# Performance work log

Measured on AMD Instinct MI355X. Metric: run time of the kernel, lower is better.

## Reference

```python
import jax, jax.numpy as jnp
import numpy as np

N = 16384
K = 4096  # codebook_size
D = 512   # embedding_dim
COMMITMENT_COST = 0.25


def setup_inputs() -> dict:
    key = jax.random.key(0)
    kz, kc = jax.random.split(key)
    z = jax.random.normal(kz, (N, D), dtype=jnp.float32)
    # nn.Embedding weight init: uniform(-1/K, 1/K)
    codebook = jax.random.uniform(kc, (K, D), dtype=jnp.float32,
                                  minval=-1.0 / K, maxval=1.0 / K)
    return {"z": z, "codebook": codebook}


def reference(z, codebook):
    # squared L2 distances: [N, K]
    dists = (jnp.sum(z * z, axis=1, keepdims=True)
             + jnp.sum(codebook * codebook, axis=1)
             - 2.0 * jnp.matmul(z, codebook.T))
    idx = jnp.argmin(dists, axis=1)                 # [N]
    z_q = codebook[idx]                             # gather == one-hot @ codebook
    # straight-through estimator
    z_q_ste = z + jax.lax.stop_gradient(z_q - z)
    commitment_loss = jnp.mean((jax.lax.stop_gradient(z) - z_q) ** 2)
    codebook_loss = jnp.mean((z - jax.lax.stop_gradient(z_q)) ** 2)
    loss = codebook_loss + COMMITMENT_COST * commitment_loss
    encoding_indices = idx[:, None]                 # [N, 1] to match torch shape
    return (z_q_ste, encoding_indices, loss)
```

## Files before the change

### kernel.cpp

```cpp
#include <hip/hip_runtime.h>
#include <math.h>

#define N_ROWS 16384
#define K_CODES 4096
#define D_DIM 512
#define NCHUNK 8
#define KCHUNK (K_CODES / NCHUNK)
#define MARGIN 2.5e-3f
#define CAND_CAP 1024

typedef unsigned int uint32;
typedef unsigned short u16t;
typedef __attribute__((ext_vector_type(8))) short short8;
typedef __attribute__((ext_vector_type(4))) float f32x4;

__device__ __forceinline__ float fmul_(float a, float b) { return __fmul_rn(a, b); }
__device__ __forceinline__ float fadd_(float a, float b) { return __fadd_rn(a, b); }

__global__ void rownorm_np_kernel(const float* __restrict__ src, int nrows,
                                  float* __restrict__ out) {
    int gid = blockIdx.x * blockDim.x + threadIdx.x;
    int row = gid >> 2;
    int blk = gid & 3;
    if (row >= nrows) return;
    const float4* p = (const float4*)(src + (size_t)row * D_DIM + blk * 128);
    float4 v0 = p[0], v1 = p[1];
    float r0 = fmul_(v0.x, v0.x), r1 = fmul_(v0.y, v0.y);
    float r2 = fmul_(v0.z, v0.z), r3 = fmul_(v0.w, v0.w);
    float r4 = fmul_(v1.x, v1.x), r5 = fmul_(v1.y, v1.y);
    float r6 = fmul_(v1.z, v1.z), r7 = fmul_(v1.w, v1.w);
#pragma unroll
    for (int i = 1; i < 16; i++) {
        float4 w0 = p[2 * i], w1 = p[2 * i + 1];
        r0 = fadd_(r0, fmul_(w0.x, w0.x));
        r1 = fadd_(r1, fmul_(w0.y, w0.y));
        r2 = fadd_(r2, fmul_(w0.z, w0.z));
        r3 = fadd_(r3, fmul_(w0.w, w0.w));
        r4 = fadd_(r4, fmul_(w1.x, w1.x));
        r5 = fadd_(r5, fmul_(w1.y, w1.y));
        r6 = fadd_(r6, fmul_(w1.z, w1.z));
        r7 = fadd_(r7, fmul_(w1.w, w1.w));
    }
    float s = fadd_(fadd_(fadd_(r0, r1), fadd_(r2, r3)),
                    fadd_(fadd_(r4, r5), fadd_(r6, r7)));
    float u = __shfl_down(s, 1, 64);
    float t = fadd_(s, u);
    float w = __shfl_down(t, 2, 64);
    float tot = fadd_(t, w);
    if (blk == 0) out[row] = tot;
}

__device__ __forceinline__ u16t f2bf(float x) {
    uint32 u = __float_as_uint(x);
    return (u16t)((u + 0x7fffu + ((u >> 16) & 1u)) >> 16);
}
__global__ void cvt_bf16_kernel(const float* __restrict__ src,
                                u16t* __restrict__ dst, int n4) {
    int i = blockIdx.x * blockDim.x + threadIdx.x;
    if (i >= n4) return;
    float4 v = ((const float4*)src)[i];
    ushort4 o;
    o.x = f2bf(v.x); o.y = f2bf(v.y); o.z = f2bf(v.z); o.w = f2bf(v.w);
    ((ushort4*)dst)[i] = o;
}

#define STS 136

__global__ __launch_bounds__(256) void score_gemm_kernel(
    const u16t* __restrict__ zb, const u16t* __restrict__ cbb,
    const float* __restrict__ cnorm, u16t* __restrict__ scores) {
    __shared__ alignas(16) u16t Ab[128 * 32];
    __shared__ alignas(16) u16t Bb[128 * 32];
    __shared__ alignas(16) u16t stile[128 * STS];

    const int t = threadIdx.x;
    const int bx = blockIdx.x;
    const int by = blockIdx.y;
    const int row0 = by * 128, k0 = bx * KCHUNK;
    const int w = t >> 6, lane = t & 63;
    const int wx = w & 1, wy = w >> 1;
    const int l15 = lane & 15, quad = lane >> 4;

    for (int kt = 0; kt < 4; kt++) {
        f32x4 acc[4][4];
#pragma unroll
        for (int i = 0; i < 4; i++)
#pragma unroll
            for (int j = 0; j < 4; j++) acc[i][j] = (f32x4){0.f, 0.f, 0.f, 0.f};

        for (int dt = 0; dt < 16; dt++) {
            __syncthreads();
#pragma unroll
            for (int q = 0; q < 2; q++) {
                int s = q * 256 + t;
                const u16t* ga = zb + (size_t)(row0 + (s >> 2)) * D_DIM + dt * 32 + (s & 3) * 8;
                __builtin_amdgcn_global_load_lds(
                    (const __attribute__((address_space(1))) void*)ga,
                    (__attribute__((address_space(3))) void*)((char*)Ab + q * 4096 + w * 1024),
                    16, 0, 0);
                const u16t* gb = cbb + (size_t)(k0 + kt * 128 + (s >> 2)) * D_DIM + dt * 32 + (s & 3) * 8;
                __builtin_amdgcn_global_load_lds(
                    (const __attribute__((address_space(1))) void*)gb,
                    (__attribute__((address_space(3))) void*)((char*)Bb + q * 4096 + w * 1024),
                    16, 0, 0);
            }
            __syncthreads();
            short8 a[4], b[4];
#pragma unroll
            for (int i = 0; i < 4; i++)
                a[i] = *(const short8*)((char*)Ab + (wy * 64 + i * 16 + l15) * 64 + quad * 16);
#pragma unroll
            for (int j = 0; j < 4; j++)
                b[j] = *(const short8*)((char*)Bb + (wx * 64 + j * 16 + l15) * 64 + quad * 16);
#pragma unroll
            for (int i = 0; i < 4; i++)
#pragma unroll
                for (int j = 0; j < 4; j++)
                    acc[i][j] = __builtin_amdgcn_mfma_f32_16x16x32_bf16(a[i], b[j], acc[i][j], 0, 0, 0);
        }
#pragma unroll
        for (int j = 0; j < 4; j++) {
            int cl = wx * 64 + j * 16 + l15;
            float cn = cnorm[k0 + kt * 128 + cl];
#pragma unroll
            for (int i = 0; i < 4; i++) {
#pragma unroll
                for (int r = 0; r < 4; r++) {
                    int rl = wy * 64 + i * 16 + quad * 4 + r;
                    float s = fmaf(-2.f, acc[i][j][r], cn);
                    stile[rl * STS + cl] = f2bf(s);
                }
            }
        }
        __syncthreads();
        for (int idx = t; idx < 128 * 16; idx += 256) {
            int row = idx >> 4, seg = idx & 15;
            short8 v = *(const short8*)&stile[row * STS + seg * 8];
            *(short8*)(scores + (size_t)(row0 + row) * K_CODES + k0 + kt * 128 + seg * 8) = v;
        }
    }
}

__global__ __launch_bounds__(256) void scan_refine_kernel(
    const u16t* __restrict__ scores,
    const float* __restrict__ z, const float* __restrict__ cb,
    const float* __restrict__ zz, const float* __restrict__ cnorm,
    float* __restrict__ out_zq, float* __restrict__ out_idx,
    float* __restrict__ rowsum) {
    __shared__ float smin[256];
    __shared__ int clist[CAND_CAP];
    __shared__ int cnt;
    __shared__ float wbv[4];
    __shared__ int wbi[4];
    __shared__ float red[256];
    __shared__ int bcast;

    const int row = blockIdx.x;
    const int t = threadIdx.x;
    const int w = t >> 6, lane = t & 63;

    if (t == 0) cnt = 0;

    const u16t* srow = scores + (size_t)row * K_CODES + t * 16;
    short8 sv0 = *(const short8*)(srow);
    short8 sv1 = *(const short8*)(srow + 8);
    float f[16];
#pragma unroll
    for (int e = 0; e < 8; e++) {
        f[e]     = __uint_as_float(((uint32)(u16t)sv0[e]) << 16);
        f[e + 8] = __uint_as_float(((uint32)(u16t)sv1[e]) << 16);
    }
    float m = f[0];
#pragma unroll
    for (int e = 1; e < 16; e++) m = fminf(m, f[e]);
    smin[t] = m;
    __syncthreads();
    for (int st = 128; st; st >>= 1) {
        if (t < st) smin[t] = fminf(smin[t], smin[t + st]);
        __syncthreads();
    }
    const float thr = smin[0] + MARGIN;

#pragma unroll
    for (int e = 0; e < 16; e++) {
        if (f[e] <= thr) {
            int pos = atomicAdd(&cnt, 1);
            if (pos < CAND_CAP) clist[pos] = t * 16 + e;
        }
    }
    __syncthreads();
    const int C = cnt < CAND_CAP ? cnt : CAND_CAP;

    const float* zr = z + (size_t)row * D_DIM;
    float4 z0 = *(const float4*)(zr + lane * 8);
    float4 z1 = *(const float4*)(zr + lane * 8 + 4);
    float zzr = zz[row];

    float bv = 3.4e38f;
    int bi = 0x7fffffff;
    for (int ci = w; ci < C; ci += 4) {
        int k = clist[ci];
        const float* cr = cb + (size_t)k * D_DIM;
        float4 c0 = *(const float4*)(cr + lane * 8);
        float4 c1 = *(const float4*)(cr + lane * 8 + 4);
        float d = fmul_(z0.x, c0.x);
        d = fmaf(z0.y, c0.y, d); d = fmaf(z0.z, c0.z, d); d = fmaf(z0.w, c0.w, d);
        d = fmaf(z1.x, c1.x, d); d = fmaf(z1.y, c1.y, d);
        d = fmaf(z1.z, c1.z, d); d = fmaf(z1.w, c1.w, d);
#pragma unroll
        for (int off = 1; off < 64; off <<= 1)
            d = fadd_(d, __shfl_xor(d, off, 64));
        float dist = fmaf(-2.f, d, fadd_(zzr, cnorm[k]));
        if (dist < bv || (dist == bv && k < bi)) { bv = dist; bi = k; }
    }
    if (lane == 0) { wbv[w] = bv; wbi[w] = bi; }
    __syncthreads();
    if (t == 0) {
        float B = wbv[0]; int I = wbi[0];
#pragma unroll
        for (int i = 1; i < 4; i++) {
            float v = wbv[i]; int ii = wbi[i];
            if (v < B || (v == B && ii < I)) { B = v; I = ii; }
        }
        bcast = I;
        out_idx[row] = (float)I;
    }
    __syncthreads();
    const int K = bcast;
    const float* cq = cb + (size_t)K * D_DIM;
    float2 zv2 = *(const float2*)(zr + t * 2);
    float2 cv2 = *(const float2*)(cq + t * 2);
    float2 o;
    o.x = fadd_(zv2.x, __fsub_rn(cv2.x, zv2.x));
    o.y = fadd_(zv2.y, __fsub_rn(cv2.y, zv2.y));
    *(float2*)(out_zq + (size_t)row * D_DIM + t * 2) = o;
    float dx = zv2.x - cv2.x, dy = zv2.y - cv2.y;
    red[t] = dx * dx + dy * dy;
    __syncthreads();
    for (int st = 128; st; st >>= 1) {
        if (t < st) red[t] += red[t + st];
        __syncthreads();
    }
    if (t == 0) rowsum[row] = red[0];
}

__global__ void loss_kernel(const float* __restrict__ rowsum,
                            float* __restrict__ out_loss) {
    __shared__ float sm[256];
    float s = 0.f;
    for (int i = threadIdx.x; i < N_ROWS; i += 256) s += rowsum[i];
    sm[threadIdx.x] = s;
    __syncthreads();
    for (int st = 128; st; st >>= 1) {
        if (threadIdx.x < st) sm[threadIdx.x] += sm[threadIdx.x + st];
        __syncthreads();
    }
    if (threadIdx.x == 0)
        *out_loss = 1.25f * sm[0] / (float)(N_ROWS * D_DIM);
}

#define BM 128
#define BN 128
#define BK 16
#define TM 8
#define TN 8

__global__ __launch_bounds__(256, 4) void vq_argmin_kernel(
    const float* __restrict__ z, const float* __restrict__ cb,
    const float* __restrict__ zz, const float* __restrict__ cnorm,
    float* __restrict__ pval, int* __restrict__ pidx) {
    __shared__ float As[BK][BM + 4];
    __shared__ float Bs[BK][BN + 4];
    __shared__ float rv[BM][17];
    __shared__ int   ri[BM][17];

    const int bx = blockIdx.x;
    const int by = blockIdx.y;
    const int row0 = by * BM;
    const int k0 = bx * KCHUNK;
    const int t = threadIdx.x;
    const int tx = t & 15;
    const int ty = t >> 4;

    float minv[TM];
    int   mini[TM];
#pragma unroll
    for (int i = 0; i < TM; i++) { minv[i] = 3.4e38f; mini[i] = 0; }
    float zrow[TM];
#pragma unroll
    for (int i = 0; i < TM; i++) zrow[i] = zz[row0 + ty * TM + i];
    const int sr = t >> 1;
    const int sdq = (t & 1) * 8;

    for (int kt = 0; kt < KCHUNK / BN; kt++) {
        const int col0 = k0 + kt * BN;
        float acc[TM][TN];
#pragma unroll
        for (int i = 0; i < TM; i++)
#pragma unroll
            for (int j = 0; j < TN; j++) acc[i][j] = 0.f;
        for (int dt = 0; dt < D_DIM; dt += BK) {
            {
                const float* src = z + (size_t)(row0 + sr) * D_DIM + dt + sdq;
                float4 v0 = *(const float4*)(src);
                float4 v1 = *(const float4*)(src + 4);
                As[sdq + 0][sr] = v0.x; As[sdq + 1][sr] = v0.y;
                As[sdq + 2][sr] = v0.z; As[sdq + 3][sr] = v0.w;
                As[sdq + 4][sr] = v1.x; As[sdq + 5][sr] = v1.y;
                As[sdq + 6][sr] = v1.z; As[sdq + 7][sr] = v1.w;
                const float* srcb = cb + (size_t)(col0 + sr) * D_DIM + dt + sdq;
                float4 w0 = *(const float4*)(srcb);
                float4 w1 = *(const float4*)(srcb + 4);
                Bs[sdq + 0][sr] = w0.x; Bs[sdq + 1][sr] = w0.y;
                Bs[sdq + 2][sr] = w0.z; Bs[sdq + 3][sr] = w0.w;
                Bs[sdq + 4][sr] = w1.x; Bs[sdq + 5][sr] = w1.y;
                Bs[sdq + 6][sr] = w1.z; Bs[sdq + 7][sr] = w1.w;
            }
            __syncthreads();
#pragma unroll
            for (int d = 0; d < BK; d++) {
                float a[TM], b[TN];
#pragma unroll
                for (int i = 0; i < TM; i++) a[i] = As[d][ty * TM + i];
#pragma unroll
                for (int j = 0; j < TN; j++) b[j] = Bs[d][tx * TN + j];
#pragma unroll
                for (int i = 0; i < TM; i++)
#pragma unroll
                    for (int j = 0; j < TN; j++)
                        acc[i][j] = fmaf(a[i], b[j], acc[i][j]);
            }
            __syncthreads();
        }
#pragma unroll
        for (int j = 0; j < TN; j++) {
            const int col = col0 + tx * TN + j;
            const float cn = cnorm[col];
#pragma unroll
            for (int i = 0; i < TM; i++) {
                float s1 = fadd_(zrow[i], cn);
                float s = fmaf(-2.f, acc[i][j], s1);
                if (s < minv[i]) { minv[i] = s; mini[i] = col; }
            }
        }
    }
#pragma unroll
    for (int i = 0; i < TM; i++) {
        rv[ty * TM + i][tx] = minv[i];
        ri[ty * TM + i][tx] = mini[i];
    }
    __syncthreads();
    if (t < BM) {
        float bv = rv[t][0];
        int   bi = ri[t][0];
#pragma unroll
        for (int x = 1; x < 16; x++) {
            float v = rv[t][x]; int ii = ri[t][x];
            if (v < bv || (v == bv && ii < bi)) { bv = v; bi = ii; }
        }
        pval[(size_t)(row0 + t) * NCHUNK + bx] = bv;
        pidx[(size_t)(row0 + t) * NCHUNK + bx] = bi;
    }
}

__global__ void finalize_kernel(const float* __restrict__ z,
                                const float* __restrict__ cb,
                                const float* __restrict__ pval,
                                const int* __restrict__ pidx,
                                float* __restrict__ out_zq,
                                float* __restrict__ out_idx,
                                float* __restrict__ rowsum) {
    int row = (blockIdx.x * blockDim.x + threadIdx.x) >> 6;
    int lane = threadIdx.x & 63;
    if (row >= N_ROWS) return;
    float bv = pval[(size_t)row * NCHUNK];
    int   bi = pidx[(size_t)row * NCHUNK];
#pragma unroll
    for (int c = 1; c < NCHUNK; c++) {
        float v = pval[(size_t)row * NCHUNK + c];
        int  ii = pidx[(size_t)row * NCHUNK + c];
        if (v < bv || (v == bv && ii < bi)) { bv = v; bi = ii; }
    }
    const float4* zr = (const float4*)(z + (size_t)row * D_DIM);
    const float4* cr = (const float4*)(cb + (size_t)bi * D_DIM);
    float4* orow = (float4*)(out_zq + (size_t)row * D_DIM);
    float s = 0.f;
#pragma unroll
    for (int i = 0; i < 2; i++) {
        float4 zv = zr[i * 64 + lane];
        float4 cv = cr[i * 64 + lane];
        float4 o;
        o.x = fadd_(zv.x, __fsub_rn(cv.x, zv.x));
        o.y = fadd_(zv.y, __fsub_rn(cv.y, zv.y));
        o.z = fadd_(zv.z, __fsub_rn(cv.z, zv.z));
        o.w = fadd_(zv.w, __fsub_rn(cv.w, zv.w));
        orow[i * 64 + lane] = o;
        float dx = zv.x - cv.x, dy = zv.y - cv.y;
        float dz = zv.z - cv.z, dw = zv.w - cv.w;
        s += dx * dx + dy * dy + dz * dz + dw * dw;
    }
#pragma unroll
    for (int off = 32; off; off >>= 1) s += __shfl_down(s, off, 64);
    if (lane == 0) {
        rowsum[row] = s;
        out_idx[row] = (float)bi;
    }
}

extern "C" void kernel_launch(void* const* d_in, const int* in_sizes, int n_in,
                              void* d_out, int out_size, void* d_ws, size_t ws_size,
                              hipStream_t stream) {
    const float* z  = (const float*)d_in[0];
    const float* cb = (const float*)d_in[1];
    float* out      = (float*)d_out;
    float* out_zq   = out;
    float* out_idx  = out + (size_t)N_ROWS * D_DIM;
    float* out_loss = out_idx + N_ROWS;

    float* zz     = (float*)d_ws;
    float* cnorm  = zz + N_ROWS;
    float* rowsum = cnorm + K_CODES;
    u16t*  z_bf   = (u16t*)(rowsum + N_ROWS);
    u16t*  cb_bf  = z_bf + (size_t)N_ROWS * D_DIM;
    u16t*  scores = cb_bf + (size_t)K_CODES * D_DIM;
    const size_t WS_NEEDED = (size_t)(N_ROWS + K_CODES + N_ROWS) * 4
                           + (size_t)N_ROWS * D_DIM * 2
                           + (size_t)K_CODES * D_DIM * 2
                           + (size_t)N_ROWS * K_CODES * 2;

    if (ws_size >= WS_NEEDED) {
        cvt_bf16_kernel<<<(N_ROWS * D_DIM / 4 + 255) / 256, 256, 0, stream>>>(z, z_bf, N_ROWS * D_DIM / 4);
        cvt_bf16_kernel<<<(K_CODES * D_DIM / 4 + 255) / 256, 256, 0, stream>>>(cb, cb_bf, K_CODES * D_DIM / 4);
        rownorm_np_kernel<<<(N_ROWS * 4) / 256, 256, 0, stream>>>(z, N_ROWS, zz);
        rownorm_np_kernel<<<(K_CODES * 4) / 256, 256, 0, stream>>>(cb, K_CODES, cnorm);

        dim3 g1(NCHUNK, N_ROWS / 128);
        score_gemm_kernel<<<g1, 256, 0, stream>>>(z_bf, cb_bf, cnorm, scores);
        scan_refine_kernel<<<N_ROWS, 256, 0, stream>>>(scores, z, cb, zz, cnorm,
                                                       out_zq, out_idx, rowsum);
        loss_kernel<<<1, 256, 0, stream>>>(rowsum, out_loss);
    } else {
        float* pval = rowsum + N_ROWS;
        int*   pidx = (int*)(pval + (size_t)N_ROWS * NCHUNK);
        rownorm_np_kernel<<<(N_ROWS * 4) / 256, 256, 0, stream>>>(z, N_ROWS, zz);
        rownorm_np_kernel<<<(K_CODES * 4) / 256, 256, 0, stream>>>(cb, K_CODES, cnorm);
        dim3 g2(NCHUNK, N_ROWS / BM);
        vq_argmin_kernel<<<g2, 256, 0, stream>>>(z, cb, zz, cnorm, pval, pidx);
        finalize_kernel<<<N_ROWS / 4, 256, 0, stream>>>(z, cb, pval, pidx,
                                                        out_zq, out_idx, rowsum);
        loss_kernel<<<1, 256, 0, stream>>>(rowsum, out_loss);
    }
}
```

Baseline: 287.5 us.

## Fuse bf16 conversion into rownorm, remap GEMM blocks per XCD, wave-per-row refine

Merges the bf16 conversion kernels into the row-norm kernel so each input is read once. The score GEMM uses a 1-D grid remapped so each XCD gets a contiguous block of tiles for L2 reuse, and halves its score staging tile by writing out in two 64-row halves. The refine kernel now assigns one row per wave and uses ballot/shuffle candidate enumeration instead of shared-memory atomics and block barriers. The GEMM adds extra syncs per tile, and the refine loop runs serially within each wave.

```diff
diff --git a/kernel.cpp b/kernel.cpp
--- a/kernel.cpp
+++ b/kernel.cpp
@@ -7,7 +7,6 @@
 #define NCHUNK 8
 #define KCHUNK (K_CODES / NCHUNK)
 #define MARGIN 2.5e-3f
-#define CAND_CAP 1024
 
 typedef unsigned int uint32;
 typedef unsigned short u16t;
@@ -17,14 +16,31 @@
 __device__ __forceinline__ float fmul_(float a, float b) { return __fmul_rn(a, b); }
 __device__ __forceinline__ float fadd_(float a, float b) { return __fadd_rn(a, b); }
 
-__global__ void rownorm_np_kernel(const float* __restrict__ src, int nrows,
-                                  float* __restrict__ out) {
+__device__ __forceinline__ u16t f2bf(float x) {
+    uint32 u = __float_as_uint(x);
+    return (u16t)((u + 0x7fffu + ((u >> 16) & 1u)) >> 16);
+}
+__device__ __forceinline__ float bf2f(u16t b) {
+    return __uint_as_float(((uint32)b) << 16);
+}
+
+__global__ void rownorm_cvt_kernel(const float* __restrict__ src, int nrows,
+                                   float* __restrict__ out,
+                                   u16t* __restrict__ bf) {
     int gid = blockIdx.x * blockDim.x + threadIdx.x;
     int row = gid >> 2;
     int blk = gid & 3;
     if (row >= nrows) return;
-    const float4* p = (const float4*)(src + (size_t)row * D_DIM + blk * 128);
+    const size_t base = (size_t)row * D_DIM + blk * 128;
+    const float4* p = (const float4*)(src + base);
     float4 v0 = p[0], v1 = p[1];
+    if (bf) {
+        ushort4 o0, o1;
+        o0.x = f2bf(v0.x); o0.y = f2bf(v0.y); o0.z = f2bf(v0.z); o0.w = f2bf(v0.w);
+        o1.x = f2bf(v1.x); o1.y = f2bf(v1.y); o1.z = f2bf(v1.z); o1.w = f2bf(v1.w);
+        *(ushort4*)(bf + base) = o0;
+        *(ushort4*)(bf + base + 4) = o1;
+    }
     float r0 = fmul_(v0.x, v0.x), r1 = fmul_(v0.y, v0.y);
     float r2 = fmul_(v0.z, v0.z), r3 = fmul_(v0.w, v0.w);
     float r4 = fmul_(v1.x, v1.x), r5 = fmul_(v1.y, v1.y);
@@ -32,6 +48,13 @@
 #pragma unroll
     for (int i = 1; i < 16; i++) {
         float4 w0 = p[2 * i], w1 = p[2 * i + 1];
+        if (bf) {
+            ushort4 o0, o1;
+            o0.x = f2bf(w0.x); o0.y = f2bf(w0.y); o0.z = f2bf(w0.z); o0.w = f2bf(w0.w);
+            o1.x = f2bf(w1.x); o1.y = f2bf(w1.y); o1.z = f2bf(w1.z); o1.w = f2bf(w1.w);
+            *(ushort4*)(bf + base + i * 8) = o0;
+            *(ushort4*)(bf + base + i * 8 + 4) = o1;
+        }
         r0 = fadd_(r0, fmul_(w0.x, w0.x));
         r1 = fadd_(r1, fmul_(w0.y, w0.y));
         r2 = fadd_(r2, fmul_(w0.z, w0.z));
@@ -50,20 +73,6 @@
     if (blk == 0) out[row] = tot;
 }
 
-__device__ __forceinline__ u16t f2bf(float x) {
-    uint32 u = __float_as_uint(x);
-    return (u16t)((u + 0x7fffu + ((u >> 16) & 1u)) >> 16);
-}
-__global__ void cvt_bf16_kernel(const float* __restrict__ src,
-                                u16t* __restrict__ dst, int n4) {
-    int i = blockIdx.x * blockDim.x + threadIdx.x;
-    if (i >= n4) return;
-    float4 v = ((const float4*)src)[i];
-    ushort4 o;
-    o.x = f2bf(v.x); o.y = f2bf(v.y); o.z = f2bf(v.z); o.w = f2bf(v.w);
-    ((ushort4*)dst)[i] = o;
-}
-
 #define STS 136
 
 __global__ __launch_bounds__(256) void score_gemm_kernel(
@@ -71,11 +80,13 @@
     const float* __restrict__ cnorm, u16t* __restrict__ scores) {
     __shared__ alignas(16) u16t Ab[128 * 32];
     __shared__ alignas(16) u16t Bb[128 * 32];
-    __shared__ alignas(16) u16t stile[128 * STS];
+    __shared__ alignas(16) u16t stile[64 * STS];
 
     const int t = threadIdx.x;
-    const int bx = blockIdx.x;
-    const int by = blockIdx.y;
+    const int id = blockIdx.x;
+    const int xcd = id & 7, q = id >> 3;
+    const int bx = ((xcd & 3) << 1) | (q >> 6);
+    const int by = ((xcd >> 2) << 6) | (q & 63);
     const int row0 = by * 128, k0 = bx * KCHUNK;
     const int w = t >> 6, lane = t & 63;
     const int wx = w & 1, wy = w >> 1;
@@ -91,17 +102,17 @@
         for (int dt = 0; dt < 16; dt++) {
             __syncthreads();
 #pragma unroll
-            for (int q = 0; q < 2; q++) {
-                int s = q * 256 + t;
+            for (int qq = 0; qq < 2; qq++) {
+                int s = qq * 256 + t;
                 const u16t* ga = zb + (size_t)(row0 + (s >> 2)) * D_DIM + dt * 32 + (s & 3) * 8;
                 __builtin_amdgcn_global_load_lds(
                     (const __attribute__((address_space(1))) void*)ga,
-                    (__attribute__((address_space(3))) void*)((char*)Ab + q * 4096 + w * 1024),
+                    (__attribute__((address_space(3))) void*)((char*)Ab + qq * 4096 + w * 1024),
                     16, 0, 0);
                 const u16t* gb = cbb + (size_t)(k0 + kt * 128 + (s >> 2)) * D_DIM + dt * 32 + (s & 3) * 8;
                 __builtin_amdgcn_global_load_lds(
                     (const __attribute__((address_space(1))) void*)gb,
-                    (__attribute__((address_space(3))) void*)((char*)Bb + q * 4096 + w * 1024),
+                    (__attribute__((address_space(3))) void*)((char*)Bb + qq * 4096 + w * 1024),
                     16, 0, 0);
             }
             __syncthreads();
@@ -119,129 +130,124 @@
                     acc[i][j] = __builtin_amdgcn_mfma_f32_16x16x32_bf16(a[i], b[j], acc[i][j], 0, 0, 0);
         }
 #pragma unroll
-        for (int j = 0; j < 4; j++) {
-            int cl = wx * 64 + j * 16 + l15;
-            float cn = cnorm[k0 + kt * 128 + cl];
-#pragma unroll
-            for (int i = 0; i < 4; i++) {
-#pragma unroll
-                for (int r = 0; r < 4; r++) {
-                    int rl = wy * 64 + i * 16 + quad * 4 + r;
-                    float s = fmaf(-2.f, acc[i][j][r], cn);
-                    stile[rl * STS + cl] = f2bf(s);
+        for (int h = 0; h < 2; h++) {
+            if (wy == h) {
+#pragma unroll
+                for (int j = 0; j < 4; j++) {
+                    int cl = wx * 64 + j * 16 + l15;
+                    float cn = cnorm[k0 + kt * 128 + cl];
+#pragma unroll
+                    for (int i = 0; i < 4; i++) {
+#pragma unroll
+                        for (int r = 0; r < 4; r++) {
+                            int rl2 = i * 16 + quad * 4 + r;
+                            float s = fmaf(-2.f, acc[i][j][r], cn);
+                            stile[rl2 * STS + cl] = f2bf(s);
+                        }
+                    }
                 }
             }
-        }
-        __syncthreads();
-        for (int idx = t; idx < 128 * 16; idx += 256) {
-            int row = idx >> 4, seg = idx & 15;
-            short8 v = *(const short8*)&stile[row * STS + seg * 8];
-            *(short8*)(scores + (size_t)(row0 + row) * K_CODES + k0 + kt * 128 + seg * 8) = v;
-        }
-    }
-}
-
-__global__ __launch_bounds__(256) void scan_refine_kernel(
+            __syncthreads();
+            for (int idx = t; idx < 64 * 16; idx += 256) {
+                int rr = idx >> 4, seg = idx & 15;
+                short8 v = *(const short8*)&stile[rr * STS + seg * 8];
+                *(short8*)(scores + (size_t)(row0 + h * 64 + rr) * K_CODES
+                           + k0 + kt * 128 + seg * 8) = v;
+            }
+            __syncthreads();
+        }
+    }
+}
+
+__global__ __launch_bounds__(256) void scan_refine_wave_kernel(
     const u16t* __restrict__ scores,
     const float* __restrict__ z, const float* __restrict__ cb,
     const float* __restrict__ zz, const float* __restrict__ cnorm,
     float* __restrict__ out_zq, float* __restrict__ out_idx,
     float* __restrict__ rowsum) {
-    __shared__ float smin[256];
-    __shared__ int clist[CAND_CAP];
-    __shared__ int cnt;
-    __shared__ float wbv[4];
-    __shared__ int wbi[4];
-    __shared__ float red[256];
-    __shared__ int bcast;
-
-    const int row = blockIdx.x;
     const int t = threadIdx.x;
     const int w = t >> 6, lane = t & 63;
-
-    if (t == 0) cnt = 0;
-
-    const u16t* srow = scores + (size_t)row * K_CODES + t * 16;
-    short8 sv0 = *(const short8*)(srow);
-    short8 sv1 = *(const short8*)(srow + 8);
-    float f[16];
-#pragma unroll
-    for (int e = 0; e < 8; e++) {
-        f[e]     = __uint_as_float(((uint32)(u16t)sv0[e]) << 16);
-        f[e + 8] = __uint_as_float(((uint32)(u16t)sv1[e]) << 16);
-    }
-    float m = f[0];
-#pragma unroll
-    for (int e = 1; e < 16; e++) m = fminf(m, f[e]);
-    smin[t] = m;
-    __syncthreads();
-    for (int st = 128; st; st >>= 1) {
-        if (t < st) smin[t] = fminf(smin[t], smin[t + st]);
-        __syncthreads();
-    }
-    const float thr = smin[0] + MARGIN;
-
-#pragma unroll
-    for (int e = 0; e < 16; e++) {
-        if (f[e] <= thr) {
-            int pos = atomicAdd(&cnt, 1);
-            if (pos < CAND_CAP) clist[pos] = t * 16 + e;
-        }
-    }
-    __syncthreads();
-    const int C = cnt < CAND_CAP ? cnt : CAND_CAP;
+    const int row = blockIdx.x * 4 + w;
+
+    const u16t* srow = scores + (size_t)row * K_CODES;
+    short8 sv[8];
+#pragma unroll
+    for (int p = 0; p < 8; p++)
+        sv[p] = *(const short8*)(srow + p * 512 + lane * 8);
+
+    float m = 3.4e38f;
+#pragma unroll
+    for (int p = 0; p < 8; p++)
+#pragma unroll
+        for (int e = 0; e < 8; e++)
+            m = fminf(m, bf2f((u16t)sv[p][e]));
+#pragma unroll
+    for (int off = 1; off < 64; off <<= 1)
+        m = fminf(m, __shfl_xor(m, off, 64));
+    const float thr = m + MARGIN;
 
     const float* zr = z + (size_t)row * D_DIM;
     float4 z0 = *(const float4*)(zr + lane * 8);
     float4 z1 = *(const float4*)(zr + lane * 8 + 4);
-    float zzr = zz[row];
+    const float zzr = zz[row];
 
     float bv = 3.4e38f;
     int bi = 0x7fffffff;
-    for (int ci = w; ci < C; ci += 4) {
-        int k = clist[ci];
-        const float* cr = cb + (size_t)k * D_DIM;
-        float4 c0 = *(const float4*)(cr + lane * 8);
-        float4 c1 = *(const float4*)(cr + lane * 8 + 4);
-        float d = fmul_(z0.x, c0.x);
-        d = fmaf(z0.y, c0.y, d); d = fmaf(z0.z, c0.z, d); d = fmaf(z0.w, c0.w, d);
-        d = fmaf(z1.x, c1.x, d); d = fmaf(z1.y, c1.y, d);
-        d = fmaf(z1.z, c1.z, d); d = fmaf(z1.w, c1.w, d);
-#pragma unroll
-        for (int off = 1; off < 64; off <<= 1)
-            d = fadd_(d, __shfl_xor(d, off, 64));
-        float dist = fmaf(-2.f, d, fadd_(zzr, cnorm[k]));
-        if (dist < bv || (dist == bv && k < bi)) { bv = dist; bi = k; }
-    }
-    if (lane == 0) { wbv[w] = bv; wbi[w] = bi; }
-    __syncthreads();
-    if (t == 0) {
-        float B = wbv[0]; int I = wbi[0];
-#pragma unroll
-        for (int i = 1; i < 4; i++) {
-            float v = wbv[i]; int ii = wbi[i];
-            if (v < B || (v == B && ii < I)) { B = v; I = ii; }
-        }
-        bcast = I;
-        out_idx[row] = (float)I;
-    }
-    __syncthreads();
-    const int K = bcast;
-    const float* cq = cb + (size_t)K * D_DIM;
-    float2 zv2 = *(const float2*)(zr + t * 2);
-    float2 cv2 = *(const float2*)(cq + t * 2);
-    float2 o;
-    o.x = fadd_(zv2.x, __fsub_rn(cv2.x, zv2.x));
-    o.y = fadd_(zv2.y, __fsub_rn(cv2.y, zv2.y));
-    *(float2*)(out_zq + (size_t)row * D_DIM + t * 2) = o;
-    float dx = zv2.x - cv2.x, dy = zv2.y - cv2.y;
-    red[t] = dx * dx + dy * dy;
-    __syncthreads();
-    for (int st = 128; st; st >>= 1) {
-        if (t < st) red[t] += red[t + st];
-        __syncthreads();
-    }
-    if (t == 0) rowsum[row] = red[0];
+#pragma unroll
+    for (int p = 0; p < 8; p++) {
+        uint32 lm = 0u;
+#pragma unroll
+        for (int e = 0; e < 8; e++)
+            if (bf2f((u16t)sv[p][e]) <= thr) lm |= (1u << e);
+        unsigned long long act = __ballot(lm != 0u);
+        while (act) {
+            int src = __ffsll(act) - 1;
+            act &= act - 1;
+            uint32 mb = (uint32)__shfl((int)lm, src, 64);
+            while (mb) {
+                int e = __ffs(mb) - 1;
+                mb &= mb - 1;
+                int k = p * 512 + src * 8 + e;
+                const float* cr = cb + (size_t)k * D_DIM;
+                float4 c0 = *(const float4*)(cr + lane * 8);
+                float4 c1 = *(const float4*)(cr + lane * 8 + 4);
+                float d = fmul_(z0.x, c0.x);
+                d = fmaf(z0.y, c0.y, d); d = fmaf(z0.z, c0.z, d); d = fmaf(z0.w, c0.w, d);
+                d = fmaf(z1.x, c1.x, d); d = fmaf(z1.y, c1.y, d);
+                d = fmaf(z1.z, c1.z, d); d = fmaf(z1.w, c1.w, d);
+#pragma unroll
+                for (int off = 1; off < 64; off <<= 1)
+                    d = fadd_(d, __shfl_xor(d, off, 64));
+                float dist = fmaf(-2.f, d, fadd_(zzr, cnorm[k]));
+                if (dist < bv || (dist == bv && k < bi)) { bv = dist; bi = k; }
+            }
+        }
+    }
+    const float* cq = cb + (size_t)bi * D_DIM;
+    float4 c0 = *(const float4*)(cq + lane * 8);
+    float4 c1 = *(const float4*)(cq + lane * 8 + 4);
+    float4 o0, o1;
+    o0.x = fadd_(z0.x, __fsub_rn(c0.x, z0.x));
+    o0.y = fadd_(z0.y, __fsub_rn(c0.y, z0.y));
+    o0.z = fadd_(z0.z, __fsub_rn(c0.z, z0.z));
+    o0.w = fadd_(z0.w, __fsub_rn(c0.w, z0.w));
+    o1.x = fadd_(z1.x, __fsub_rn(c1.x, z1.x));
+    o1.y = fadd_(z1.y, __fsub_rn(c1.y, z1.y));
+    o1.z = fadd_(z1.z, __fsub_rn(c1.z, z1.z));
+    o1.w = fadd_(z1.w, __fsub_rn(c1.w, z1.w));
+    float* orow = out_zq + (size_t)row * D_DIM + lane * 8;
+    *(float4*)(orow) = o0;
+    *(float4*)(orow + 4) = o1;
+    float dx0 = z0.x - c0.x, dy0 = z0.y - c0.y, dz0 = z0.z - c0.z, dw0 = z0.w - c0.w;
+    float dx1 = z1.x - c1.x, dy1 = z1.y - c1.y, dz1 = z1.z - c1.z, dw1 = z1.w - c1.w;
+    float s = dx0 * dx0 + dy0 * dy0 + dz0 * dz0 + dw0 * dw0
+            + dx1 * dx1 + dy1 * dy1 + dz1 * dz1 + dw1 * dw1;
+#pragma unroll
+    for (int off = 32; off; off >>= 1) s += __shfl_down(s, off, 64);
+    if (lane == 0) {
+        rowsum[row] = s;
+        out_idx[row] = (float)bi;
+    }
 }
 
 __global__ void loss_kernel(const float* __restrict__ rowsum,
@@ -429,21 +435,18 @@
                            + (size_t)N_ROWS * K_CODES * 2;
 
     if (ws_size >= WS_NEEDED) {
-        cvt_bf16_kernel<<<(N_ROWS * D_DIM / 4 + 255) / 256, 256, 0, stream>>>(z, z_bf, N_ROWS * D_DIM / 4);
-        cvt_bf16_kernel<<<(K_CODES * D_DIM / 4 + 255) / 256, 256, 0, stream>>>(cb, cb_bf, K_CODES * D_DIM / 4);
-        rownorm_np_kernel<<<(N_ROWS * 4) / 256, 256, 0, stream>>>(z, N_ROWS, zz);
-        rownorm_np_kernel<<<(K_CODES * 4) / 256, 256, 0, stream>>>(cb, K_CODES, cnorm);
-
-        dim3 g1(NCHUNK, N_ROWS / 128);
-        score_gemm_kernel<<<g1, 256, 0, stream>>>(z_bf, cb_bf, cnorm, scores);
-        scan_refine_kernel<<<N_ROWS, 256, 0, stream>>>(scores, z, cb, zz, cnorm,
-                                                       out_zq, out_idx, rowsum);
+        rownorm_cvt_kernel<<<(N_ROWS * 4) / 256, 256, 0, stream>>>(z, N_ROWS, zz, z_bf);
+        rownorm_cvt_kernel<<<(K_CODES * 4) / 256, 256, 0, stream>>>(cb, K_CODES, cnorm, cb_bf);
+
+        score_gemm_kernel<<<NCHUNK * (N_ROWS / 128), 256, 0, stream>>>(z_bf, cb_bf, cnorm, scores);
+        scan_refine_wave_kernel<<<N_ROWS / 4, 256, 0, stream>>>(scores, z, cb, zz, cnorm,
+                                                                out_zq, out_idx, rowsum);
         loss_kernel<<<1, 256, 0, stream>>>(rowsum, out_loss);
     } else {
         float* pval = rowsum + N_ROWS;
         int*   pidx = (int*)(pval + (size_t)N_ROWS * NCHUNK);
-        rownorm_np_kernel<<<(N_ROWS * 4) / 256, 256, 0, stream>>>(z, N_ROWS, zz);
-        rownorm_np_kernel<<<(K_CODES * 4) / 256, 256, 0, stream>>>(cb, K_CODES, cnorm);
+        rownorm_cvt_kernel<<<(N_ROWS * 4) / 256, 256, 0, stream>>>(z, N_ROWS, zz, (u16t*)0);
+        rownorm_cvt_kernel<<<(K_CODES * 4) / 256, 256, 0, stream>>>(cb, K_CODES, cnorm, (u16t*)0);
         dim3 g2(NCHUNK, N_ROWS / BM);
         vq_argmin_kernel<<<g2, 256, 0, stream>>>(z, cb, zz, cnorm, pval, pidx);
         finalize_kernel<<<N_ROWS / 4, 256, 0, stream>>>(z, cb, pval, pidx,
```

Result: slower. 312.3 us (+8.6%).
